# Kernel tuning notes

Measured on AMD Instinct MI355X. Metric: run time of the kernel, lower is better.

The kernel has to match this reference:

```python
import jax, jax.numpy as jnp
import numpy as np

N, D = 65536, 64            # flattened batch, state dim (size_in)
G, K = 4, 512               # number of gammas, components per gamma


def setup_inputs() -> dict:
    key = jax.random.key(0)
    k1, k2 = jax.random.split(key)
    states = jax.random.normal(k1, (N, D), dtype=jnp.float32)
    centers = jax.random.normal(k2, (G, K, D), dtype=jnp.float32)  # RBF centers, one bank per gamma
    gammas = jnp.array([0.5, 1.0, 2.0, 5.0], dtype=jnp.float32)
    return {"states": states, "centers": centers, "gammas": gammas}


def reference(states, centers, gammas):
    # states: [N, D]; centers: [G, K, D]; gammas: [G]
    x2 = jnp.sum(states * states, axis=-1)            # [N]
    c2 = jnp.sum(centers * centers, axis=-1)          # [G, K]
    xc = jnp.einsum('nd,gkd->gnk', states, centers)   # [G, N, K]
    d2 = x2[None, :, None] + c2[:, None, :] - 2.0 * xc  # [G, N, K]
    d2 = jnp.maximum(d2, 0.0)
    feats = jnp.exp(-gammas[:, None, None] * d2)      # [G, N, K]
    # concatenate per-gamma feature banks along feature dim -> [N, G*K]
    out = jnp.moveaxis(feats, 0, 1).reshape(states.shape[0], -1)
    return out
```

## Files before the change

kernel.cpp:

```cpp
#include <hip/hip_runtime.h>
#include <math.h>

#define N_TOT 65536
#define D_DIM 64
#define G_NUM 4
#define K_NUM 512
#define BM 128
#define BN 128

typedef __attribute__((ext_vector_type(4))) float  f32x4;
typedef __attribute__((ext_vector_type(8))) short  short8;

__device__ __forceinline__ unsigned int f2u(float x)        { return __builtin_bit_cast(unsigned int, x); }
__device__ __forceinline__ float        u2f(unsigned int x) { return __builtin_bit_cast(float, x); }

__device__ __forceinline__ unsigned int bf_rne(float x) {
    unsigned int u = f2u(x);
    return (u + 0x7FFFu + ((u >> 16) & 1u)) >> 16;
}

__device__ __forceinline__ int swz(int row, int byteInRow) {
    return (row << 7) + (byteInRow ^ ((row & 7) << 4));
}

#define AHI_OFF 0
#define ALO_OFF 16384
#define BHI_OFF 32768
#define BLO_OFF 49152

__global__ void rowsq64_kernel(const float* __restrict__ in,
                               float* __restrict__ out, int nrows) {
    int gtid = blockIdx.x * blockDim.x + threadIdx.x;
    int row  = gtid >> 6;
    int lane = threadIdx.x & 63;
    if (row >= nrows) return;
    float v = in[(size_t)row * D_DIM + lane];
    float s = v * v;
    #pragma unroll
    for (int off = 32; off > 0; off >>= 1)
        s += __shfl_xor(s, off, 64);
    if (lane == 0) out[row] = s;
}

__global__ __launch_bounds__(256, 2)
void rbf_mfma_kernel(const float* __restrict__ states,
                     const float* __restrict__ centers,
                     const float* __restrict__ gammas,
                     const float* __restrict__ x2,
                     const float* __restrict__ c2,
                     float* __restrict__ out)
{
    __shared__ __align__(16) unsigned char lds[65536];

    const int tid = threadIdx.x;
    const int n0  = blockIdx.x * BM;
    const int k0  = blockIdx.y * BN;
    const int g   = blockIdx.z;

    {
        const int r0 = tid >> 4;
        const int cc = tid & 15;
        #pragma unroll
        for (int i = 0; i < 8; ++i) {
            const int row = r0 + 16 * i;
            const float4 av = *(const float4*)(states  + (size_t)(n0 + row) * D_DIM + 4 * cc);
            const float4 bv = *(const float4*)(centers + ((size_t)g * K_NUM + (size_t)(k0 + row)) * D_DIM + 4 * cc);
            const int wb = swz(row, 8 * cc);

            {
                unsigned h0 = f2u(av.x) & 0xFFFF0000u, h1 = f2u(av.y) & 0xFFFF0000u;
                unsigned h2 = f2u(av.z) & 0xFFFF0000u, h3 = f2u(av.w) & 0xFFFF0000u;
                uint2 hi = make_uint2((h0 >> 16) | h1, (h2 >> 16) | h3);
                uint2 lo = make_uint2(bf_rne(av.x - u2f(h0)) | (bf_rne(av.y - u2f(h1)) << 16),
                                      bf_rne(av.z - u2f(h2)) | (bf_rne(av.w - u2f(h3)) << 16));
                *(uint2*)(lds + AHI_OFF + wb) = hi;
                *(uint2*)(lds + ALO_OFF + wb) = lo;
            }
            {
                unsigned h0 = f2u(bv.x) & 0xFFFF0000u, h1 = f2u(bv.y) & 0xFFFF0000u;
                unsigned h2 = f2u(bv.z) & 0xFFFF0000u, h3 = f2u(bv.w) & 0xFFFF0000u;
                uint2 hi = make_uint2((h0 >> 16) | h1, (h2 >> 16) | h3);
                uint2 lo = make_uint2(bf_rne(bv.x - u2f(h0)) | (bf_rne(bv.y - u2f(h1)) << 16),
                                      bf_rne(bv.z - u2f(h2)) | (bf_rne(bv.w - u2f(h3)) << 16));
                *(uint2*)(lds + BHI_OFF + wb) = hi;
                *(uint2*)(lds + BLO_OFF + wb) = lo;
            }
        }
    }
    __syncthreads();

    const int lane = tid & 63;
    const int w    = tid >> 6;
    const int wr   = w >> 1;
    const int wc   = w & 1;
    const int fr   = lane & 15;
    const int q    = lane >> 4;

    short8 ahi[4][2], alo[4][2];
    #pragma unroll
    for (int ms = 0; ms < 4; ++ms) {
        const int row = wr * 64 + ms * 16 + fr;
        #pragma unroll
        for (int h = 0; h < 2; ++h) {
            const int off = swz(row, 64 * h + 16 * q);
            ahi[ms][h] = *(const short8*)(lds + AHI_OFF + off);
            alo[ms][h] = *(const short8*)(lds + ALO_OFF + off);
        }
    }

    f32x4 acc[4][4];
    #pragma unroll
    for (int ms = 0; ms < 4; ++ms)
        #pragma unroll
        for (int ns = 0; ns < 4; ++ns)
            acc[ms][ns] = (f32x4){0.f, 0.f, 0.f, 0.f};

    #pragma unroll
    for (int ns = 0; ns < 4; ++ns) {
        const int rowb = wc * 64 + ns * 16 + fr;
        short8 bhi[2], blo[2];
        #pragma unroll
        for (int h = 0; h < 2; ++h) {
            const int off = swz(rowb, 64 * h + 16 * q);
            bhi[h] = *(const short8*)(lds + BHI_OFF + off);
            blo[h] = *(const short8*)(lds + BLO_OFF + off);
        }
        #pragma unroll
        for (int ms = 0; ms < 4; ++ms) {
            #pragma unroll
            for (int h = 0; h < 2; ++h) {
                acc[ms][ns] = __builtin_amdgcn_mfma_f32_16x16x32_bf16(ahi[ms][h], bhi[h], acc[ms][ns], 0, 0, 0);
                acc[ms][ns] = __builtin_amdgcn_mfma_f32_16x16x32_bf16(ahi[ms][h], blo[h], acc[ms][ns], 0, 0, 0);
                acc[ms][ns] = __builtin_amdgcn_mfma_f32_16x16x32_bf16(alo[ms][h], bhi[h], acc[ms][ns], 0, 0, 0);
            }
        }
    }

    const float gamma = gammas[g];

    float x2v[4][4];
    #pragma unroll
    for (int ms = 0; ms < 4; ++ms)
        #pragma unroll
        for (int r = 0; r < 4; ++r)
            x2v[ms][r] = x2[n0 + wr * 64 + ms * 16 + 4 * q + r];

    float c2v[4];
    #pragma unroll
    for (int ns = 0; ns < 4; ++ns)
        c2v[ns] = c2[g * K_NUM + k0 + wc * 64 + ns * 16 + fr];

    #pragma unroll
    for (int ms = 0; ms < 4; ++ms) {
        #pragma unroll
        for (int ns = 0; ns < 4; ++ns) {
            const size_t col = (size_t)g * K_NUM + k0 + wc * 64 + ns * 16 + fr;
            #pragma unroll
            for (int r = 0; r < 4; ++r) {
                const int rown = n0 + wr * 64 + ms * 16 + 4 * q + r;
                float d2 = x2v[ms][r] + c2v[ns] - 2.0f * acc[ms][ns][r];
                d2 = fmaxf(d2, 0.0f);
                out[(size_t)rown * (G_NUM * K_NUM) + col] = __expf(-gamma * d2);
            }
        }
    }
}

extern "C" void kernel_launch(void* const* d_in, const int* in_sizes, int n_in,
                              void* d_out, int out_size, void* d_ws, size_t ws_size,
                              hipStream_t stream) {
    const float* states  = (const float*)d_in[0];
    const float* centers = (const float*)d_in[1];
    const float* gammas  = (const float*)d_in[2];
    float* out = (float*)d_out;

    float* x2 = (float*)d_ws;
    float* c2 = x2 + N_TOT;

    {
        int threads = 256;
        int blocks_x2 = (N_TOT * 64) / threads;
        int blocks_c2 = (G_NUM * K_NUM * 64) / threads;
        rowsq64_kernel<<<blocks_x2, threads, 0, stream>>>(states, x2, N_TOT);
        rowsq64_kernel<<<blocks_c2, threads, 0, stream>>>(centers, c2, G_NUM * K_NUM);
    }

    dim3 grid(N_TOT / BM, K_NUM / BN, G_NUM);
    rbf_mfma_kernel<<<grid, 256, 0, stream>>>(states, centers, gammas, x2, c2, out);
}
```

Measured before the change: 598.2 us.

## Pre-split operands into swizzled bf16 tiles, DMA to LDS, vectorize output stores

A prep kernel now converts states and centers once into pre-swizzled hi/lo bf16 tiles and computes the row norms in the same pass. The main kernel loads these tiles straight into LDS with global_load_lds, so each of the many blocks that reuse a tile no longer repeats the fp32-to-bf16 split. The MFMA operands are swapped so each lane's accumulator holds four consecutive output columns, which allows float4 stores to the large output instead of scalar stores. The cost is extra workspace and one more pass over the inputs to write the prepared tiles.

```diff
diff --git a/kernel.cpp b/kernel.cpp
--- a/kernel.cpp
+++ b/kernel.cpp
@@ -5,11 +5,12 @@
 #define D_DIM 64
 #define G_NUM 4
 #define K_NUM 512
-#define BM 128
-#define BN 128
 
 typedef __attribute__((ext_vector_type(4))) float  f32x4;
 typedef __attribute__((ext_vector_type(8))) short  short8;
+
+typedef const __attribute__((address_space(1))) void glb_cv;
+typedef __attribute__((address_space(3))) void lds_v;
 
 __device__ __forceinline__ unsigned int f2u(float x)        { return __builtin_bit_cast(unsigned int, x); }
 __device__ __forceinline__ float        u2f(unsigned int x) { return __builtin_bit_cast(float, x); }
@@ -28,83 +29,83 @@
 #define BHI_OFF 32768
 #define BLO_OFF 49152
 
-__global__ void rowsq64_kernel(const float* __restrict__ in,
-                               float* __restrict__ out, int nrows) {
-    int gtid = blockIdx.x * blockDim.x + threadIdx.x;
-    int row  = gtid >> 6;
-    int lane = threadIdx.x & 63;
-    if (row >= nrows) return;
-    float v = in[(size_t)row * D_DIM + lane];
-    float s = v * v;
+__global__ void prep_kernel(const float* __restrict__ in,
+                            unsigned char* __restrict__ tiles,
+                            float* __restrict__ sq, int nrows)
+{
+    int gtid = blockIdx.x * 256 + threadIdx.x;
+    if (gtid >= nrows * 8) return;
+    int row = gtid >> 3, c = gtid & 7;
+    const float* p = in + (size_t)row * D_DIM + 8 * c;
+    float4 v0 = *(const float4*)p;
+    float4 v1 = *(const float4*)(p + 4);
+    float vs[8] = {v0.x, v0.y, v0.z, v0.w, v1.x, v1.y, v1.z, v1.w};
+    unsigned hi[4], lo[4];
+    float s = 0.f;
     #pragma unroll
-    for (int off = 32; off > 0; off >>= 1)
-        s += __shfl_xor(s, off, 64);
-    if (lane == 0) out[row] = s;
+    for (int i = 0; i < 4; ++i) {
+        float a = vs[2 * i], b = vs[2 * i + 1];
+        s += a * a + b * b;
+        unsigned ha = f2u(a) & 0xFFFF0000u, hb = f2u(b) & 0xFFFF0000u;
+        hi[i] = (ha >> 16) | hb;
+        lo[i] = bf_rne(a - u2f(ha)) | (bf_rne(b - u2f(hb)) << 16);
+    }
+    int tile = row >> 7, r = row & 127;
+    int cs = c ^ (r & 7);
+    unsigned char* base = tiles + (size_t)tile * 32768 + r * 128 + cs * 16;
+    *(uint4*)(base)         = make_uint4(hi[0], hi[1], hi[2], hi[3]);
+    *(uint4*)(base + 16384) = make_uint4(lo[0], lo[1], lo[2], lo[3]);
+    s += __shfl_xor(s, 1, 64);
+    s += __shfl_xor(s, 2, 64);
+    s += __shfl_xor(s, 4, 64);
+    if (c == 0) sq[row] = s;
 }
 
 __global__ __launch_bounds__(256, 2)
-void rbf_mfma_kernel(const float* __restrict__ states,
-                     const float* __restrict__ centers,
-                     const float* __restrict__ gammas,
-                     const float* __restrict__ x2,
-                     const float* __restrict__ c2,
-                     float* __restrict__ out)
+void rbf_mfma2(const unsigned char* __restrict__ Aprep,
+               const unsigned char* __restrict__ Bprep,
+               const float* __restrict__ gammas,
+               const float* __restrict__ x2,
+               const float* __restrict__ c2,
+               float* __restrict__ out)
 {
     __shared__ __align__(16) unsigned char lds[65536];
 
     const int tid = threadIdx.x;
-    const int n0  = blockIdx.x * BM;
-    const int k0  = blockIdx.y * BN;
+    const int n0  = blockIdx.x * 128;
+    const int kt  = blockIdx.y;
     const int g   = blockIdx.z;
+    const int k0  = kt * 128;
 
-    {
-        const int r0 = tid >> 4;
-        const int cc = tid & 15;
-        #pragma unroll
-        for (int i = 0; i < 8; ++i) {
-            const int row = r0 + 16 * i;
-            const float4 av = *(const float4*)(states  + (size_t)(n0 + row) * D_DIM + 4 * cc);
-            const float4 bv = *(const float4*)(centers + ((size_t)g * K_NUM + (size_t)(k0 + row)) * D_DIM + 4 * cc);
-            const int wb = swz(row, 8 * cc);
+    const int lane = tid & 63;
+    const int w    = tid >> 6;
 
-            {
-                unsigned h0 = f2u(av.x) & 0xFFFF0000u, h1 = f2u(av.y) & 0xFFFF0000u;
-                unsigned h2 = f2u(av.z) & 0xFFFF0000u, h3 = f2u(av.w) & 0xFFFF0000u;
-                uint2 hi = make_uint2((h0 >> 16) | h1, (h2 >> 16) | h3);
-                uint2 lo = make_uint2(bf_rne(av.x - u2f(h0)) | (bf_rne(av.y - u2f(h1)) << 16),
-                                      bf_rne(av.z - u2f(h2)) | (bf_rne(av.w - u2f(h3)) << 16));
-                *(uint2*)(lds + AHI_OFF + wb) = hi;
-                *(uint2*)(lds + ALO_OFF + wb) = lo;
-            }
-            {
-                unsigned h0 = f2u(bv.x) & 0xFFFF0000u, h1 = f2u(bv.y) & 0xFFFF0000u;
-                unsigned h2 = f2u(bv.z) & 0xFFFF0000u, h3 = f2u(bv.w) & 0xFFFF0000u;
-                uint2 hi = make_uint2((h0 >> 16) | h1, (h2 >> 16) | h3);
-                uint2 lo = make_uint2(bf_rne(bv.x - u2f(h0)) | (bf_rne(bv.y - u2f(h1)) << 16),
-                                      bf_rne(bv.z - u2f(h2)) | (bf_rne(bv.w - u2f(h3)) << 16));
-                *(uint2*)(lds + BHI_OFF + wb) = hi;
-                *(uint2*)(lds + BLO_OFF + wb) = lo;
-            }
-        }
+    const unsigned char* Asrc = Aprep + (size_t)blockIdx.x * 32768;
+    const unsigned char* Bsrc = Bprep + (size_t)(g * 4 + kt) * 32768;
+    #pragma unroll
+    for (int i = 0; i < 8; ++i) {
+        const int off = w * 8192 + i * 1024;
+        __builtin_amdgcn_global_load_lds((glb_cv*)(Asrc + off + lane * 16),
+                                         (lds_v*)(lds + off), 16, 0, 0);
+        __builtin_amdgcn_global_load_lds((glb_cv*)(Bsrc + off + lane * 16),
+                                         (lds_v*)(lds + 32768 + off), 16, 0, 0);
     }
     __syncthreads();
 
-    const int lane = tid & 63;
-    const int w    = tid >> 6;
-    const int wr   = w >> 1;
-    const int wc   = w & 1;
-    const int fr   = lane & 15;
-    const int q    = lane >> 4;
+    const int wr = w >> 1;
+    const int wc = w & 1;
+    const int fr = lane & 15;
+    const int q  = lane >> 4;
 
-    short8 ahi[4][2], alo[4][2];
+    short8 xhi[4][2], xlo[4][2];
     #pragma unroll
     for (int ms = 0; ms < 4; ++ms) {
         const int row = wr * 64 + ms * 16 + fr;
         #pragma unroll
         for (int h = 0; h < 2; ++h) {
             const int off = swz(row, 64 * h + 16 * q);
-            ahi[ms][h] = *(const short8*)(lds + AHI_OFF + off);
-            alo[ms][h] = *(const short8*)(lds + ALO_OFF + off);
+            xhi[ms][h] = *(const short8*)(lds + AHI_OFF + off);
+            xlo[ms][h] = *(const short8*)(lds + ALO_OFF + off);
         }
     }
 
@@ -117,51 +118,48 @@
 
     #pragma unroll
     for (int ns = 0; ns < 4; ++ns) {
-        const int rowb = wc * 64 + ns * 16 + fr;
-        short8 bhi[2], blo[2];
+        const int rowc = wc * 64 + ns * 16 + fr;
+        short8 chi[2], clo[2];
         #pragma unroll
         for (int h = 0; h < 2; ++h) {
-            const int off = swz(rowb, 64 * h + 16 * q);
-            bhi[h] = *(const short8*)(lds + BHI_OFF + off);
-            blo[h] = *(const short8*)(lds + BLO_OFF + off);
+            const int off = swz(rowc, 64 * h + 16 * q);
+            chi[h] = *(const short8*)(lds + BHI_OFF + off);
+            clo[h] = *(const short8*)(lds + BLO_OFF + off);
         }
         #pragma unroll
         for (int ms = 0; ms < 4; ++ms) {
             #pragma unroll
             for (int h = 0; h < 2; ++h) {
-                acc[ms][ns] = __builtin_amdgcn_mfma_f32_16x16x32_bf16(ahi[ms][h], bhi[h], acc[ms][ns], 0, 0, 0);
-                acc[ms][ns] = __builtin_amdgcn_mfma_f32_16x16x32_bf16(ahi[ms][h], blo[h], acc[ms][ns], 0, 0, 0);
-                acc[ms][ns] = __builtin_amdgcn_mfma_f32_16x16x32_bf16(alo[ms][h], bhi[h], acc[ms][ns], 0, 0, 0);
+                acc[ms][ns] = __builtin_amdgcn_mfma_f32_16x16x32_bf16(chi[h], xhi[ms][h], acc[ms][ns], 0, 0, 0);
+                acc[ms][ns] = __builtin_amdgcn_mfma_f32_16x16x32_bf16(chi[h], xlo[ms][h], acc[ms][ns], 0, 0, 0);
+                acc[ms][ns] = __builtin_amdgcn_mfma_f32_16x16x32_bf16(clo[h], xhi[ms][h], acc[ms][ns], 0, 0, 0);
             }
         }
     }
 
     const float gamma = gammas[g];
 
-    float x2v[4][4];
+    float c2v[4][4];
+    const float* c2g = c2 + g * K_NUM + k0 + wc * 64;
     #pragma unroll
-    for (int ms = 0; ms < 4; ++ms)
-        #pragma unroll
-        for (int r = 0; r < 4; ++r)
-            x2v[ms][r] = x2[n0 + wr * 64 + ms * 16 + 4 * q + r];
-
-    float c2v[4];
-    #pragma unroll
-    for (int ns = 0; ns < 4; ++ns)
-        c2v[ns] = c2[g * K_NUM + k0 + wc * 64 + ns * 16 + fr];
+    for (int ns = 0; ns < 4; ++ns) {
+        float4 t = *(const float4*)(c2g + ns * 16 + 4 * q);
+        c2v[ns][0] = t.x; c2v[ns][1] = t.y; c2v[ns][2] = t.z; c2v[ns][3] = t.w;
+    }
 
     #pragma unroll
     for (int ms = 0; ms < 4; ++ms) {
+        const int n = n0 + wr * 64 + ms * 16 + fr;
+        const float xv = x2[n];
+        float* rowp = out + (size_t)n * (G_NUM * K_NUM) + (size_t)g * K_NUM + k0 + wc * 64;
         #pragma unroll
         for (int ns = 0; ns < 4; ++ns) {
-            const size_t col = (size_t)g * K_NUM + k0 + wc * 64 + ns * 16 + fr;
-            #pragma unroll
-            for (int r = 0; r < 4; ++r) {
-                const int rown = n0 + wr * 64 + ms * 16 + 4 * q + r;
-                float d2 = x2v[ms][r] + c2v[ns] - 2.0f * acc[ms][ns][r];
-                d2 = fmaxf(d2, 0.0f);
-                out[(size_t)rown * (G_NUM * K_NUM) + col] = __expf(-gamma * d2);
-            }
+            float4 o;
+            o.x = __expf(-gamma * fmaxf(xv + c2v[ns][0] - 2.0f * acc[ms][ns][0], 0.f));
+            o.y = __expf(-gamma * fmaxf(xv + c2v[ns][1] - 2.0f * acc[ms][ns][1], 0.f));
+            o.z = __expf(-gamma * fmaxf(xv + c2v[ns][2] - 2.0f * acc[ms][ns][2], 0.f));
+            o.w = __expf(-gamma * fmaxf(xv + c2v[ns][3] - 2.0f * acc[ms][ns][3], 0.f));
+            *(float4*)(rowp + ns * 16 + 4 * q) = o;
         }
     }
 }
@@ -174,17 +172,14 @@
     const float* gammas  = (const float*)d_in[2];
     float* out = (float*)d_out;
 
-    float* x2 = (float*)d_ws;
+    unsigned char* Aprep = (unsigned char*)d_ws;
+    unsigned char* Bprep = Aprep + (size_t)512 * 32768;
+    float* x2 = (float*)(Bprep + (size_t)16 * 32768);
     float* c2 = x2 + N_TOT;
 
-    {
-        int threads = 256;
-        int blocks_x2 = (N_TOT * 64) / threads;
-        int blocks_c2 = (G_NUM * K_NUM * 64) / threads;
-        rowsq64_kernel<<<blocks_x2, threads, 0, stream>>>(states, x2, N_TOT);
-        rowsq64_kernel<<<blocks_c2, threads, 0, stream>>>(centers, c2, G_NUM * K_NUM);
-    }
+    prep_kernel<<<(N_TOT * 8) / 256, 256, 0, stream>>>(states, Aprep, x2, N_TOT);
+    prep_kernel<<<(G_NUM * K_NUM * 8) / 256, 256, 0, stream>>>(centers, Bprep, c2, G_NUM * K_NUM);
 
-    dim3 grid(N_TOT / BM, K_NUM / BN, G_NUM);
-    rbf_mfma_kernel<<<grid, 256, 0, stream>>>(states, centers, gammas, x2, c2, out);
+    dim3 grid(N_TOT / 128, K_NUM / 128, G_NUM);
+    rbf_mfma2<<<grid, 256, 0, stream>>>(Aprep, Bprep, gammas, x2, c2, out);
 }
```

After: 589.5 us. About the same (-1.5%).
